# Performance work log

Hardware: AMD Instinct MI355X
Metric: run time of the kernel (lower is better)

## Reference

```python
import jax, jax.numpy as jnp
import numpy as np

B, H = 8192, 768


def _mk_linear(key, fan_in, fan_out):
    k1, k2 = jax.random.split(key)
    lim = 1.0 / np.sqrt(fan_in)
    W = jax.random.uniform(k1, (fan_out, fan_in), jnp.float32, -lim, lim)
    b = jax.random.uniform(k2, (fan_out,), jnp.float32, -lim, lim)
    return W, b


def setup_inputs() -> dict:
    key = jax.random.key(0)
    ks = jax.random.split(key, 6)
    modal_a = jax.random.normal(ks[0], (B, H), jnp.float32)
    modal_b = jax.random.normal(ks[1], (B, H), jnp.float32)
    W1m, b1m = _mk_linear(ks[2], H, H)
    W2m, b2m = _mk_linear(ks[3], H, H)
    W1v, b1v = _mk_linear(ks[4], H, H)
    W2v, b2v = _mk_linear(ks[5], H, H)
    return {"modal_a": modal_a, "modal_b": modal_b,
            "W1m": W1m, "b1m": b1m, "W2m": W2m, "b2m": b2m,
            "W1v": W1v, "b1v": b1v, "W2v": W2v, "b2v": b2v}


def reference(modal_a, modal_b, W1m, b1m, W2m, b2m, W1v, b1v, W2v, b2v):
    # mlp_mu: Linear -> Tanh -> Linear
    mu = jnp.tanh(modal_a @ W1m.T + b1m) @ W2m.T + b2m              # [B,H]
    # mlp_logvar: Linear -> Tanh -> Linear -> Tanh
    logvar = jnp.tanh(jnp.tanh(modal_a @ W1v.T + b1v) @ W2v.T + b2v)  # [B,H]
    inv_var = jnp.exp(-logvar)

    positive = -(mu - modal_b) ** 2 * 0.5 * inv_var                  # [B,H]

    # mean_j (mu[j] - mu[i])^2 = E[mu^2] - 2*mu[i]*E[mu] + mu[i]^2  (per feature dim)
    # Algebraic reduction of the O(B^2*H) tile in the original code.
    mu_mean = jnp.mean(mu, axis=0)                                   # [H]
    mu_sq_mean = jnp.mean(mu * mu, axis=0)                           # [H]
    pair_sq = mu_sq_mean - 2.0 * mu * mu_mean + mu * mu              # [B,H]
    negative = -pair_sq * 0.5 * inv_var                              # [B,H]

    pos_sum = jnp.sum(positive, axis=-1)                             # [B]
    neg_sum = jnp.sum(negative, axis=-1)                             # [B]
    lld = jnp.mean(pos_sum)
    bound = jnp.mean(pos_sum - neg_sum)
    return (lld, bound)
```

## Files before the change

kernel.cpp:

```cpp
#include <hip/hip_runtime.h>
#include <math.h>

typedef float v4f __attribute__((ext_vector_type(4)));
typedef short bf16x8 __attribute__((ext_vector_type(8)));

#define AS1 __attribute__((address_space(1)))
#define AS3 __attribute__((address_space(3)))

static constexpr int Bn = 8192;
static constexpr int Hn = 768;
static constexpr float invB = 1.0f / 8192.0f;

__device__ __forceinline__ short f32_to_bf16(float x) {
    union { float f; unsigned u; } v; v.f = x;
    unsigned r = (v.u + 0x7FFFu + ((v.u >> 16) & 1u)) >> 16;
    return (short)r;
}

__device__ __forceinline__ float fast_tanh(float x) {
    float xc = fminf(fmaxf(x, -15.0f), 15.0f);
    float e = __expf(2.0f * xc);
    float r = __builtin_amdgcn_rcpf(e + 1.0f);
    return 1.0f - 2.0f * r;
}

__global__ void prep_kernel(const float* __restrict__ A,
                            const float* __restrict__ W1m, const float* __restrict__ W2m,
                            const float* __restrict__ W1v, const float* __restrict__ W2v,
                            short* __restrict__ A_bf,
                            short* __restrict__ W1m_bf, short* __restrict__ W2m_bf,
                            short* __restrict__ W1v_bf, short* __restrict__ W2v_bf,
                            float* __restrict__ zbuf, int nzero) {
    const int tid = blockIdx.x * blockDim.x + threadIdx.x;
    if (tid < nzero) zbuf[tid] = 0.0f;
    constexpr int A4 = Bn * Hn / 4;
    constexpr int W4 = Hn * Hn / 4;
    const int total = A4 + 4 * W4;
    const int stride = gridDim.x * blockDim.x;
    for (int i = tid; i < total; i += stride) {
        const float* s; short* d; int j;
        if (i < A4) { s = A; d = A_bf; j = i; }
        else {
            int k = i - A4; int w = k / W4; j = k - w * W4;
            s = (w == 0) ? W1m : (w == 1) ? W2m : (w == 2) ? W1v : W2v;
            d = (w == 0) ? W1m_bf : (w == 1) ? W2m_bf : (w == 2) ? W1v_bf : W2v_bf;
        }
        float4 v = ((const float4*)s)[j];
        short4 o;
        o.x = f32_to_bf16(v.x); o.y = f32_to_bf16(v.y);
        o.z = f32_to_bf16(v.z); o.w = f32_to_bf16(v.w);
        ((short4*)d)[j] = o;
    }
}

template <int LAYER>
__launch_bounds__(256, 5)
__global__ void gemm_club(const short* __restrict__ Am_g, const short* __restrict__ Av_g,
                          const short* __restrict__ Wm_g, const short* __restrict__ Wv_g,
                          const float* __restrict__ bm, const float* __restrict__ bv,
                          short* __restrict__ outm, short* __restrict__ outv,
                          const float* __restrict__ mb,
                          float* __restrict__ cs, float* __restrict__ cs2,
                          float* __restrict__ siv, float* __restrict__ sivmu,
                          float* __restrict__ accum) {
    constexpr int K = Hn;
    constexpr int NSH = (LAYER == 1) ? 3 * 4096 : 4 * 4096;
    __shared__ __align__(16) short smem[NSH];
    short* As_m = smem;
    short* As_v = (LAYER == 1) ? smem : smem + 4096;
    short* Ws_m = (LAYER == 1) ? smem + 4096 : smem + 8192;
    short* Ws_v = (LAYER == 1) ? smem + 8192 : smem + 12288;

    const int t = threadIdx.x;
    const int row0 = blockIdx.x * 64;
    const int col0 = blockIdx.y * 64;
    const int w = t >> 6, lane = t & 63;
    const int wm = w >> 1, wn = w & 1;
    const int lr = lane & 15, quad = lane >> 4;

    const int rt = t >> 3;
    const int bsrc = (t & 7) ^ (rt & 7);

    const short* pAm[2]; const short* pAv[2]; const short* pWm[2]; const short* pWv[2];
#pragma unroll
    for (int i = 0; i < 2; ++i) {
        pAm[i] = Am_g + (size_t)(row0 + i * 32 + rt) * K + bsrc * 8;
        pWm[i] = Wm_g + (size_t)(col0 + i * 32 + rt) * K + bsrc * 8;
        pWv[i] = Wv_g + (size_t)(col0 + i * 32 + rt) * K + bsrc * 8;
        pAv[i] = (LAYER == 2) ? (Av_g + (size_t)(row0 + i * 32 + rt) * K + bsrc * 8) : pAm[i];
    }

    v4f accm[2][2] = {}, accv[2][2] = {};

    for (int k0 = 0; k0 < K; k0 += 64) {
#pragma unroll
        for (int i = 0; i < 2; ++i) {
            __builtin_amdgcn_global_load_lds((AS1 void*)pAm[i], (AS3 void*)&As_m[i * 2048 + t * 8], 16, 0, 0);
            if (LAYER == 2)
                __builtin_amdgcn_global_load_lds((AS1 void*)pAv[i], (AS3 void*)&As_v[i * 2048 + t * 8], 16, 0, 0);
            __builtin_amdgcn_global_load_lds((AS1 void*)pWm[i], (AS3 void*)&Ws_m[i * 2048 + t * 8], 16, 0, 0);
            __builtin_amdgcn_global_load_lds((AS1 void*)pWv[i], (AS3 void*)&Ws_v[i * 2048 + t * 8], 16, 0, 0);
            pAm[i] += 64; pWm[i] += 64; pWv[i] += 64;
            if (LAYER == 2) pAv[i] += 64;
        }
        __syncthreads();
#pragma unroll
        for (int s = 0; s < 2; ++s) {
            const int kb = s * 4 + quad;
            bf16x8 am[2], av[2], bmf[2], bvf[2];
#pragma unroll
            for (int mt = 0; mt < 2; ++mt) {
                int m = wm * 32 + mt * 16 + lr;
                int off = m * 64 + ((kb ^ (m & 7)) << 3);
                am[mt] = *(const bf16x8*)&As_m[off];
                if (LAYER == 2) av[mt] = *(const bf16x8*)&As_v[off];
            }
#pragma unroll
            for (int nt = 0; nt < 2; ++nt) {
                int n = wn * 32 + nt * 16 + lr;
                int off = n * 64 + ((kb ^ (n & 7)) << 3);
                bmf[nt] = *(const bf16x8*)&Ws_m[off];
                bvf[nt] = *(const bf16x8*)&Ws_v[off];
            }
#pragma unroll
            for (int mt = 0; mt < 2; ++mt)
#pragma unroll
                for (int nt = 0; nt < 2; ++nt) {
                    accm[mt][nt] = __builtin_amdgcn_mfma_f32_16x16x32_bf16(am[mt], bmf[nt], accm[mt][nt], 0, 0, 0);
                    accv[mt][nt] = __builtin_amdgcn_mfma_f32_16x16x32_bf16(
                        (LAYER == 1) ? am[mt] : av[mt], bvf[nt], accv[mt][nt], 0, 0, 0);
                }
        }
        __syncthreads();
    }

    if (LAYER == 1) {
#pragma unroll
        for (int nt = 0; nt < 2; ++nt) {
            const int col = col0 + wn * 32 + nt * 16 + lr;
            const float bmc = bm[col], bvc = bv[col];
#pragma unroll
            for (int mt = 0; mt < 2; ++mt) {
#pragma unroll
                for (int r = 0; r < 4; ++r) {
                    const int row = row0 + wm * 32 + mt * 16 + quad * 4 + r;
                    outm[(size_t)row * Hn + col] = f32_to_bf16(fast_tanh(accm[mt][nt][r] + bmc));
                    outv[(size_t)row * Hn + col] = f32_to_bf16(fast_tanh(accv[mt][nt][r] + bvc));
                }
            }
        }
    } else {
        float pos = 0.f, q = 0.f;
#pragma unroll
        for (int nt = 0; nt < 2; ++nt) {
            const int col = col0 + wn * 32 + nt * 16 + lr;
            const float bmc = bm[col], bvc = bv[col];
            float c1 = 0.f, c2 = 0.f, c3 = 0.f, c4 = 0.f;
#pragma unroll
            for (int mt = 0; mt < 2; ++mt) {
#pragma unroll
                for (int r = 0; r < 4; ++r) {
                    const int row = row0 + wm * 32 + mt * 16 + quad * 4 + r;
                    float mu = accm[mt][nt][r] + bmc;
                    float tv = fast_tanh(accv[mt][nt][r] + bvc);
                    float iv = __expf(-tv);
                    float mbv = mb[(size_t)row * Hn + col];
                    float d = mu - mbv;
                    pos += iv * d * d;
                    q   += iv * mu * mu;
                    c1 += mu; c2 += mu * mu; c3 += iv; c4 += iv * mu;
                }
            }
            c1 += __shfl_xor(c1, 16); c1 += __shfl_xor(c1, 32);
            c2 += __shfl_xor(c2, 16); c2 += __shfl_xor(c2, 32);
            c3 += __shfl_xor(c3, 16); c3 += __shfl_xor(c3, 32);
            c4 += __shfl_xor(c4, 16); c4 += __shfl_xor(c4, 32);
            if (quad == 0) {
                atomicAdd(&cs[col], c1);
                atomicAdd(&cs2[col], c2);
                atomicAdd(&siv[col], c3);
                atomicAdd(&sivmu[col], c4);
            }
        }
        for (int off = 32; off > 0; off >>= 1) {
            pos += __shfl_down(pos, off);
            q   += __shfl_down(q, off);
        }
        __shared__ float redP[4], redQ[4];
        if (lane == 0) { redP[w] = pos; redQ[w] = q; }
        __syncthreads();
        if (t == 0) {
            atomicAdd(&accum[0], redP[0] + redP[1] + redP[2] + redP[3]);
            atomicAdd(&accum[1], redQ[0] + redQ[1] + redQ[2] + redQ[3]);
        }
    }
}

__global__ void combine_kernel(const float* __restrict__ cs, const float* __restrict__ cs2,
                               const float* __restrict__ siv, const float* __restrict__ sivmu,
                               const float* __restrict__ accum, float* __restrict__ out) {
    const int h = threadIdx.x;
    float term = siv[h] * cs2[h] - 2.0f * sivmu[h] * cs[h];
    for (int off = 32; off > 0; off >>= 1) term += __shfl_down(term, off);
    __shared__ float red[12];
    const int lane = h & 63, w = h >> 6;
    if (lane == 0) red[w] = term;
    __syncthreads();
    if (h == 0) {
        float T = 0.f;
#pragma unroll
        for (int i = 0; i < 12; ++i) T += red[i];
        float P = accum[0];
        float Q = accum[1];
        float pos_sum = -0.5f * P;
        float neg_sum = -0.5f * (T * invB + Q);
        out[0] = pos_sum * invB;
        out[1] = (pos_sum - neg_sum) * invB;
    }
}

extern "C" void kernel_launch(void* const* d_in, const int* in_sizes, int n_in,
                              void* d_out, int out_size, void* d_ws, size_t ws_size,
                              hipStream_t stream) {
    const float* modal_a = (const float*)d_in[0];
    const float* modal_b = (const float*)d_in[1];
    const float* W1m = (const float*)d_in[2];
    const float* b1m = (const float*)d_in[3];
    const float* W2m = (const float*)d_in[4];
    const float* b2m = (const float*)d_in[5];
    const float* W1v = (const float*)d_in[6];
    const float* b1v = (const float*)d_in[7];
    const float* W2v = (const float*)d_in[8];
    const float* b2v = (const float*)d_in[9];
    float* out = (float*)d_out;

    char* ws = (char*)d_ws;
    constexpr size_t szAH = (size_t)Bn * Hn * 2;
    constexpr size_t szW  = (size_t)Hn * Hn * 2;
    short* A_bf   = (short*)(ws);
    short* h1m    = (short*)(ws + szAH);
    short* h1v    = (short*)(ws + 2 * szAH);
    short* W1m_bf = (short*)(ws + 3 * szAH);
    short* W2m_bf = (short*)(ws + 3 * szAH + szW);
    short* W1v_bf = (short*)(ws + 3 * szAH + 2 * szW);
    short* W2v_bf = (short*)(ws + 3 * szAH + 3 * szW);
    float* cs     = (float*)(ws + 3 * szAH + 4 * szW);
    float* cs2    = cs + Hn;
    float* siv    = cs + 2 * Hn;
    float* sivmu  = cs + 3 * Hn;
    float* accum  = cs + 4 * Hn;

    prep_kernel<<<1280, 256, 0, stream>>>(modal_a, W1m, W2m, W1v, W2v,
                                          A_bf, W1m_bf, W2m_bf, W1v_bf, W2v_bf,
                                          cs, 4 * Hn + 2);

    dim3 grid(Bn / 64, Hn / 64);
    gemm_club<1><<<grid, 256, 0, stream>>>(A_bf, A_bf, W1m_bf, W1v_bf, b1m, b1v,
                                           h1m, h1v, nullptr,
                                           nullptr, nullptr, nullptr, nullptr, nullptr);

    gemm_club<2><<<grid, 256, 0, stream>>>(h1m, h1v, W2m_bf, W2v_bf, b2m, b2v,
                                           nullptr, nullptr, modal_b,
                                           cs, cs2, siv, sivmu, accum);

    combine_kernel<<<1, 768, 0, stream>>>(cs, cs2, siv, sivmu, accum, out);
}
```

Measured before the change: 197.3 us.

## Enlarge GEMM tiles to 128x128 with 32x32x16 MFMA and split layer-1 branches

Both GEMM layers move from 64x64 block tiles using 16x16x32 MFMA to 128x128 tiles using 32x32x16 MFMA. Each wave now computes a 64x64 sub-tile, which raises arithmetic intensity and cuts global and LDS traffic per FLOP. Layer 1 no longer computes the mu and logvar branches in one block; it uses a z-dimension of 2, one branch per block. The cost is more accumulator registers, more LDS per block, lower occupancy and fewer blocks (384 for layer 2), and the epilogue's atomic reductions now cover larger tiles.

```diff
diff --git a/kernel.cpp b/kernel.cpp
--- a/kernel.cpp
+++ b/kernel.cpp
@@ -1,7 +1,7 @@
 #include <hip/hip_runtime.h>
 #include <math.h>
 
-typedef float v4f __attribute__((ext_vector_type(4)));
+typedef float v16f __attribute__((ext_vector_type(16)));
 typedef short bf16x8 __attribute__((ext_vector_type(8)));
 
 #define AS1 __attribute__((address_space(1)))
@@ -53,71 +53,144 @@
     }
 }
 
-template <int LAYER>
-__launch_bounds__(256, 5)
-__global__ void gemm_club(const short* __restrict__ Am_g, const short* __restrict__ Av_g,
-                          const short* __restrict__ Wm_g, const short* __restrict__ Wv_g,
-                          const float* __restrict__ bm, const float* __restrict__ bv,
-                          short* __restrict__ outm, short* __restrict__ outv,
-                          const float* __restrict__ mb,
-                          float* __restrict__ cs, float* __restrict__ cs2,
-                          float* __restrict__ siv, float* __restrict__ sivmu,
-                          float* __restrict__ accum) {
+__launch_bounds__(256, 3)
+__global__ void gemm_l1(const short* __restrict__ A_g,
+                        const short* __restrict__ Wm_g, const short* __restrict__ Wv_g,
+                        const float* __restrict__ bm, const float* __restrict__ bv,
+                        short* __restrict__ outm, short* __restrict__ outv) {
     constexpr int K = Hn;
-    constexpr int NSH = (LAYER == 1) ? 3 * 4096 : 4 * 4096;
-    __shared__ __align__(16) short smem[NSH];
-    short* As_m = smem;
-    short* As_v = (LAYER == 1) ? smem : smem + 4096;
-    short* Ws_m = (LAYER == 1) ? smem + 4096 : smem + 8192;
-    short* Ws_v = (LAYER == 1) ? smem + 8192 : smem + 12288;
+    __shared__ __align__(16) short As[128 * 64];
+    __shared__ __align__(16) short Ws[128 * 64];
+
+    const int z = blockIdx.z;
+    const short* W = z ? Wv_g : Wm_g;
+    const float* bias = z ? bv : bm;
+    short* out = z ? outv : outm;
 
     const int t = threadIdx.x;
-    const int row0 = blockIdx.x * 64;
-    const int col0 = blockIdx.y * 64;
+    const int row0 = blockIdx.x * 128;
+    const int col0 = blockIdx.y * 128;
     const int w = t >> 6, lane = t & 63;
     const int wm = w >> 1, wn = w & 1;
-    const int lr = lane & 15, quad = lane >> 4;
+    const int lc = lane & 31, lh = lane >> 5;
 
     const int rt = t >> 3;
     const int bsrc = (t & 7) ^ (rt & 7);
 
-    const short* pAm[2]; const short* pAv[2]; const short* pWm[2]; const short* pWv[2];
-#pragma unroll
-    for (int i = 0; i < 2; ++i) {
+    const short* pA[4]; const short* pW[4];
+#pragma unroll
+    for (int i = 0; i < 4; ++i) {
+        pA[i] = A_g + (size_t)(row0 + i * 32 + rt) * K + bsrc * 8;
+        pW[i] = W + (size_t)(col0 + i * 32 + rt) * K + bsrc * 8;
+    }
+
+    v16f acc[2][2] = {};
+
+    for (int k0 = 0; k0 < K; k0 += 64) {
+#pragma unroll
+        for (int i = 0; i < 4; ++i) {
+            __builtin_amdgcn_global_load_lds((AS1 void*)pA[i], (AS3 void*)&As[i * 2048 + t * 8], 16, 0, 0);
+            __builtin_amdgcn_global_load_lds((AS1 void*)pW[i], (AS3 void*)&Ws[i * 2048 + t * 8], 16, 0, 0);
+            pA[i] += 64; pW[i] += 64;
+        }
+        __syncthreads();
+#pragma unroll
+        for (int ks = 0; ks < 4; ++ks) {
+            const int kb = ks * 2 + lh;
+            bf16x8 af[2], bfr[2];
+#pragma unroll
+            for (int mt = 0; mt < 2; ++mt) {
+                int m = wm * 64 + mt * 32 + lc;
+                af[mt] = *(const bf16x8*)&As[m * 64 + ((kb ^ (m & 7)) << 3)];
+            }
+#pragma unroll
+            for (int nt = 0; nt < 2; ++nt) {
+                int n = wn * 64 + nt * 32 + lc;
+                bfr[nt] = *(const bf16x8*)&Ws[n * 64 + ((kb ^ (n & 7)) << 3)];
+            }
+#pragma unroll
+            for (int mt = 0; mt < 2; ++mt)
+#pragma unroll
+                for (int nt = 0; nt < 2; ++nt)
+                    acc[mt][nt] = __builtin_amdgcn_mfma_f32_32x32x16_bf16(af[mt], bfr[nt], acc[mt][nt], 0, 0, 0);
+        }
+        __syncthreads();
+    }
+
+#pragma unroll
+    for (int nt = 0; nt < 2; ++nt) {
+        const int col = col0 + wn * 64 + nt * 32 + lc;
+        const float bc = bias[col];
+#pragma unroll
+        for (int mt = 0; mt < 2; ++mt) {
+#pragma unroll
+            for (int reg = 0; reg < 16; ++reg) {
+                const int row = row0 + wm * 64 + mt * 32 + (reg & 3) + 8 * (reg >> 2) + 4 * lh;
+                out[(size_t)row * Hn + col] = f32_to_bf16(fast_tanh(acc[mt][nt][reg] + bc));
+            }
+        }
+    }
+}
+
+__launch_bounds__(256, 2)
+__global__ void gemm_l2(const short* __restrict__ Am_g, const short* __restrict__ Av_g,
+                        const short* __restrict__ Wm_g, const short* __restrict__ Wv_g,
+                        const float* __restrict__ bm, const float* __restrict__ bv,
+                        const float* __restrict__ mb,
+                        float* __restrict__ cs, float* __restrict__ cs2,
+                        float* __restrict__ siv, float* __restrict__ sivmu,
+                        float* __restrict__ accum) {
+    constexpr int K = Hn;
+    __shared__ __align__(16) short As_m[128 * 64];
+    __shared__ __align__(16) short As_v[128 * 64];
+    __shared__ __align__(16) short Ws_m[128 * 64];
+    __shared__ __align__(16) short Ws_v[128 * 64];
+
+    const int t = threadIdx.x;
+    const int row0 = blockIdx.x * 128;
+    const int col0 = blockIdx.y * 128;
+    const int w = t >> 6, lane = t & 63;
+    const int wm = w >> 1, wn = w & 1;
+    const int lc = lane & 31, lh = lane >> 5;
+
+    const int rt = t >> 3;
+    const int bsrc = (t & 7) ^ (rt & 7);
+
+    const short* pAm[4]; const short* pAv[4]; const short* pWm[4]; const short* pWv[4];
+#pragma unroll
+    for (int i = 0; i < 4; ++i) {
         pAm[i] = Am_g + (size_t)(row0 + i * 32 + rt) * K + bsrc * 8;
+        pAv[i] = Av_g + (size_t)(row0 + i * 32 + rt) * K + bsrc * 8;
         pWm[i] = Wm_g + (size_t)(col0 + i * 32 + rt) * K + bsrc * 8;
         pWv[i] = Wv_g + (size_t)(col0 + i * 32 + rt) * K + bsrc * 8;
-        pAv[i] = (LAYER == 2) ? (Av_g + (size_t)(row0 + i * 32 + rt) * K + bsrc * 8) : pAm[i];
-    }
-
-    v4f accm[2][2] = {}, accv[2][2] = {};
+    }
+
+    v16f accm[2][2] = {}, accv[2][2] = {};
 
     for (int k0 = 0; k0 < K; k0 += 64) {
 #pragma unroll
-        for (int i = 0; i < 2; ++i) {
+        for (int i = 0; i < 4; ++i) {
             __builtin_amdgcn_global_load_lds((AS1 void*)pAm[i], (AS3 void*)&As_m[i * 2048 + t * 8], 16, 0, 0);
-            if (LAYER == 2)
-                __builtin_amdgcn_global_load_lds((AS1 void*)pAv[i], (AS3 void*)&As_v[i * 2048 + t * 8], 16, 0, 0);
+            __builtin_amdgcn_global_load_lds((AS1 void*)pAv[i], (AS3 void*)&As_v[i * 2048 + t * 8], 16, 0, 0);
             __builtin_amdgcn_global_load_lds((AS1 void*)pWm[i], (AS3 void*)&Ws_m[i * 2048 + t * 8], 16, 0, 0);
             __builtin_amdgcn_global_load_lds((AS1 void*)pWv[i], (AS3 void*)&Ws_v[i * 2048 + t * 8], 16, 0, 0);
-            pAm[i] += 64; pWm[i] += 64; pWv[i] += 64;
-            if (LAYER == 2) pAv[i] += 64;
+            pAm[i] += 64; pAv[i] += 64; pWm[i] += 64; pWv[i] += 64;
         }
         __syncthreads();
 #pragma unroll
-        for (int s = 0; s < 2; ++s) {
-            const int kb = s * 4 + quad;
+        for (int ks = 0; ks < 4; ++ks) {
+            const int kb = ks * 2 + lh;
             bf16x8 am[2], av[2], bmf[2], bvf[2];
 #pragma unroll
             for (int mt = 0; mt < 2; ++mt) {
-                int m = wm * 32 + mt * 16 + lr;
+                int m = wm * 64 + mt * 32 + lc;
                 int off = m * 64 + ((kb ^ (m & 7)) << 3);
                 am[mt] = *(const bf16x8*)&As_m[off];
-                if (LAYER == 2) av[mt] = *(const bf16x8*)&As_v[off];
+                av[mt] = *(const bf16x8*)&As_v[off];
             }
 #pragma unroll
             for (int nt = 0; nt < 2; ++nt) {
-                int n = wn * 32 + nt * 16 + lr;
+                int n = wn * 64 + nt * 32 + lc;
                 int off = n * 64 + ((kb ^ (n & 7)) << 3);
                 bmf[nt] = *(const bf16x8*)&Ws_m[off];
                 bvf[nt] = *(const bf16x8*)&Ws_v[off];
@@ -126,73 +199,53 @@
             for (int mt = 0; mt < 2; ++mt)
 #pragma unroll
                 for (int nt = 0; nt < 2; ++nt) {
-                    accm[mt][nt] = __builtin_amdgcn_mfma_f32_16x16x32_bf16(am[mt], bmf[nt], accm[mt][nt], 0, 0, 0);
-                    accv[mt][nt] = __builtin_amdgcn_mfma_f32_16x16x32_bf16(
-                        (LAYER == 1) ? am[mt] : av[mt], bvf[nt], accv[mt][nt], 0, 0, 0);
+                    accm[mt][nt] = __builtin_amdgcn_mfma_f32_32x32x16_bf16(am[mt], bmf[nt], accm[mt][nt], 0, 0, 0);
+                    accv[mt][nt] = __builtin_amdgcn_mfma_f32_32x32x16_bf16(av[mt], bvf[nt], accv[mt][nt], 0, 0, 0);
                 }
         }
         __syncthreads();
     }
 
-    if (LAYER == 1) {
-#pragma unroll
-        for (int nt = 0; nt < 2; ++nt) {
-            const int col = col0 + wn * 32 + nt * 16 + lr;
-            const float bmc = bm[col], bvc = bv[col];
-#pragma unroll
-            for (int mt = 0; mt < 2; ++mt) {
-#pragma unroll
-                for (int r = 0; r < 4; ++r) {
-                    const int row = row0 + wm * 32 + mt * 16 + quad * 4 + r;
-                    outm[(size_t)row * Hn + col] = f32_to_bf16(fast_tanh(accm[mt][nt][r] + bmc));
-                    outv[(size_t)row * Hn + col] = f32_to_bf16(fast_tanh(accv[mt][nt][r] + bvc));
-                }
-            }
-        }
-    } else {
-        float pos = 0.f, q = 0.f;
-#pragma unroll
-        for (int nt = 0; nt < 2; ++nt) {
-            const int col = col0 + wn * 32 + nt * 16 + lr;
-            const float bmc = bm[col], bvc = bv[col];
-            float c1 = 0.f, c2 = 0.f, c3 = 0.f, c4 = 0.f;
-#pragma unroll
-            for (int mt = 0; mt < 2; ++mt) {
-#pragma unroll
-                for (int r = 0; r < 4; ++r) {
-                    const int row = row0 + wm * 32 + mt * 16 + quad * 4 + r;
-                    float mu = accm[mt][nt][r] + bmc;
-                    float tv = fast_tanh(accv[mt][nt][r] + bvc);
-                    float iv = __expf(-tv);
-                    float mbv = mb[(size_t)row * Hn + col];
-                    float d = mu - mbv;
-                    pos += iv * d * d;
-                    q   += iv * mu * mu;
-                    c1 += mu; c2 += mu * mu; c3 += iv; c4 += iv * mu;
-                }
-            }
-            c1 += __shfl_xor(c1, 16); c1 += __shfl_xor(c1, 32);
-            c2 += __shfl_xor(c2, 16); c2 += __shfl_xor(c2, 32);
-            c3 += __shfl_xor(c3, 16); c3 += __shfl_xor(c3, 32);
-            c4 += __shfl_xor(c4, 16); c4 += __shfl_xor(c4, 32);
-            if (quad == 0) {
-                atomicAdd(&cs[col], c1);
-                atomicAdd(&cs2[col], c2);
-                atomicAdd(&siv[col], c3);
-                atomicAdd(&sivmu[col], c4);
-            }
-        }
-        for (int off = 32; off > 0; off >>= 1) {
-            pos += __shfl_down(pos, off);
-            q   += __shfl_down(q, off);
-        }
-        __shared__ float redP[4], redQ[4];
-        if (lane == 0) { redP[w] = pos; redQ[w] = q; }
-        __syncthreads();
-        if (t == 0) {
-            atomicAdd(&accum[0], redP[0] + redP[1] + redP[2] + redP[3]);
-            atomicAdd(&accum[1], redQ[0] + redQ[1] + redQ[2] + redQ[3]);
-        }
+    float pos = 0.f, q = 0.f;
+#pragma unroll
+    for (int nt = 0; nt < 2; ++nt) {
+        const int col = col0 + wn * 64 + nt * 32 + lc;
+        const float bmc = bm[col], bvc = bv[col];
+        float c1 = 0.f, c2 = 0.f, c3 = 0.f, c4 = 0.f;
+#pragma unroll
+        for (int mt = 0; mt < 2; ++mt) {
+#pragma unroll
+            for (int reg = 0; reg < 16; ++reg) {
+                const int row = row0 + wm * 64 + mt * 32 + (reg & 3) + 8 * (reg >> 2) + 4 * lh;
+                float mu = accm[mt][nt][reg] + bmc;
+                float tv = fast_tanh(accv[mt][nt][reg] + bvc);
+                float iv = __expf(-tv);
+                float mbv = mb[(size_t)row * Hn + col];
+                float d = mu - mbv;
+                pos += iv * d * d;
+                q   += iv * mu * mu;
+                c1 += mu; c2 += mu * mu; c3 += iv; c4 += iv * mu;
+            }
+        }
+        c1 += __shfl_xor(c1, 32); c2 += __shfl_xor(c2, 32);
+        c3 += __shfl_xor(c3, 32); c4 += __shfl_xor(c4, 32);
+        if (lh == 0) {
+            atomicAdd(&cs[col], c1);
+            atomicAdd(&cs2[col], c2);
+            atomicAdd(&siv[col], c3);
+            atomicAdd(&sivmu[col], c4);
+        }
+    }
+    for (int off = 32; off > 0; off >>= 1) {
+        pos += __shfl_down(pos, off);
+        q   += __shfl_down(q, off);
+    }
+    __shared__ float redP[4], redQ[4];
+    if (lane == 0) { redP[w] = pos; redQ[w] = q; }
+    __syncthreads();
+    if (t == 0) {
+        atomicAdd(&accum[0], redP[0] + redP[1] + redP[2] + redP[3]);
+        atomicAdd(&accum[1], redQ[0] + redQ[1] + redQ[2] + redQ[3]);
     }
 }
 
@@ -254,14 +307,12 @@
                                           A_bf, W1m_bf, W2m_bf, W1v_bf, W2v_bf,
                                           cs, 4 * Hn + 2);
 
-    dim3 grid(Bn / 64, Hn / 64);
-    gemm_club<1><<<grid, 256, 0, stream>>>(A_bf, A_bf, W1m_bf, W1v_bf, b1m, b1v,
-                                           h1m, h1v, nullptr,
-                                           nullptr, nullptr, nullptr, nullptr, nullptr);
-
-    gemm_club<2><<<grid, 256, 0, stream>>>(h1m, h1v, W2m_bf, W2v_bf, b2m, b2v,
-                                           nullptr, nullptr, modal_b,
-                                           cs, cs2, siv, sivmu, accum);
+    gemm_l1<<<dim3(Bn / 128, Hn / 128, 2), 256, 0, stream>>>(
+        A_bf, W1m_bf, W1v_bf, b1m, b1v, h1m, h1v);
+
+    gemm_l2<<<dim3(Bn / 128, Hn / 128), 256, 0, stream>>>(
+        h1m, h1v, W2m_bf, W2v_bf, b2m, b2v, modal_b,
+        cs, cs2, siv, sivmu, accum);
 
     combine_kernel<<<1, 768, 0, stream>>>(cs, cs2, siv, sivmu, accum, out);
 }
```

Result: faster. 180.8 us (-8.4%).
